# Optimization experiments

Hardware: AMD Instinct MI355X
Metric: run time of the kernel (lower is better)

The kernel has to match this reference:

```python
import jax, jax.numpy as jnp
import numpy as np

L, D, HID, NH, E, K, P, IMG, NC, B = 4, 384, 1536, 6, 8, 2, 16, 224, 1000, 8
S = (IMG // P) ** 2 + 1  # 197 tokens (cls + patches)
EPS = 1e-5


def setup_inputs() -> dict:
    ks = iter(jax.random.split(jax.random.key(0), 32))
    g = lambda shape, s=0.02: jax.random.normal(next(ks), shape, jnp.float32) * s
    pd = 3 * P * P
    return dict(
        x=jax.random.normal(next(ks), (B, 3, IMG, IMG), jnp.float32),
        patch_w=g((pd, D)), patch_b=g((D,)),
        cls_tok=g((1, 1, D)), pos=g((1, S, D)),
        qkv_w=g((L, D, 3 * D)), qkv_b=g((L, 3 * D)),
        proj_w=g((L, D, D)), proj_b=g((L, D)),
        ln1_g=jnp.ones((L, D)), ln1_b=jnp.zeros((L, D)),
        ln2_g=jnp.ones((L, D)), ln2_b=jnp.zeros((L, D)),
        router_w=g((L, D, E)), router_b=g((L, E)),
        w1=g((L, E, D, HID)), b1=g((L, E, HID)),
        w2=g((L, E, HID, D)), b2=g((L, E, D)),
        norm_g=jnp.ones((D,)), norm_b=jnp.zeros((D,)),
        fc_w=g((D, NC)), fc_b=g((NC,)),
    )


def _ln(x, g, b):
    m = x.mean(-1, keepdims=True)
    v = ((x - m) ** 2).mean(-1, keepdims=True)
    return (x - m) * jax.lax.rsqrt(v + EPS) * g + b


def _mha(x, wqkv, bqkv, wo, bo):
    Bx, Sx, Dx = x.shape
    hd = Dx // NH
    qkv = x @ wqkv + bqkv
    q, k, v = jnp.split(qkv, 3, axis=-1)
    q = q.reshape(Bx, Sx, NH, hd)
    k = k.reshape(Bx, Sx, NH, hd)
    v = v.reshape(Bx, Sx, NH, hd)
    att = jnp.einsum('bqhd,bkhd->bhqk', q, k) / jnp.sqrt(jnp.float32(hd))
    att = jax.nn.softmax(att, axis=-1)
    o = jnp.einsum('bhqk,bkhd->bqhd', att, v).reshape(Bx, Sx, Dx)
    return o @ wo + bo


def _moe(x, rw, rb, w1, b1, w2, b2, noise):
    # Faithful to the masked-dense SparseMoE: non-routed experts see zeros,
    # so occupied experts leak expert_j(0)=gelu(b1_j)@W2_j+b2_j to all tokens.
    xf = x.reshape(-1, x.shape[-1])                     # [T, D]
    logits = xf @ rw + rb + noise * 0.01                # noisy gating
    vals, idx = jax.lax.top_k(logits, K)                # [T, K]
    gates = jax.nn.softmax(vals, axis=-1)               # [T, K]
    h = jax.nn.gelu(jnp.einsum('td,edh->teh', xf, w1) + b1[None], approximate=False)
    y = jnp.einsum('teh,ehd->ted', h, w2) + b2[None]    # [T, E, D]
    bias0 = jnp.einsum('eh,ehd->ed', jax.nn.gelu(b1, approximate=False), w2) + b2  # expert_j(0)
    oh = jax.nn.one_hot(idx, E, dtype=xf.dtype)         # [T, K, E]
    occ = (oh.sum(0) > 0).astype(xf.dtype)              # [K, E] slot occupancy (mask.sum()>0)
    bias_sum = occ @ bias0                              # [K, D]
    y_sel = jnp.take_along_axis(y, idx[:, :, None], axis=1)  # [T, K, D]
    out = jnp.einsum('tk,tkd->td', gates, y_sel - bias0[idx] + bias_sum[None])
    return out.reshape(x.shape)


def reference(x, patch_w, patch_b, cls_tok, pos, qkv_w, qkv_b, proj_w, proj_b,
              ln1_g, ln1_b, ln2_g, ln2_b, router_w, router_b,
              w1, b1, w2, b2, norm_g, norm_b, fc_w, fc_b):
    Bx = x.shape[0]
    Hp = IMG // P
    # torch unfold patchify: (B,C,Hp,Wp,p,p) -> (B, N, C*p*p), channel-major features
    patches = x.reshape(Bx, 3, Hp, P, Hp, P).transpose(0, 2, 4, 1, 3, 5).reshape(Bx, Hp * Hp, 3 * P * P)
    t = patches @ patch_w + patch_b
    t = jnp.concatenate([jnp.broadcast_to(cls_tok, (Bx, 1, D)), t], axis=1) + pos
    nkey = jax.random.key(42)
    for l in range(L):
        a = _mha(t, qkv_w[l], qkv_b[l], proj_w[l], proj_b[l])
        t = _ln(t + a, ln1_g[l], ln1_b[l])
        noise = jax.random.normal(jax.random.fold_in(nkey, l), (Bx * S, E), t.dtype)
        m = _moe(t, router_w[l], router_b[l], w1[l], b1[l], w2[l], b2[l], noise)
        t = _ln(t + m, ln2_g[l], ln2_b[l])
    t = _ln(t, norm_g, norm_b)
    return t[:, 0] @ fc_w + fc_b
```

## Files before the change

kernel.cpp:

```cpp
#include <hip/hip_runtime.h>
#include <hip/hip_bf16.h>

constexpr int LYR  = 4;
constexpr int DM   = 384;
constexpr int HIDN = 1536;
constexpr int NHEAD = 6;
constexpr int HDIM = 64;
constexpr int NEXP = 8;
constexpr int SEQ  = 197;
constexpr int BATCH = 8;
constexpr int TOK  = BATCH * SEQ;
constexpr int NCLS = 1000;
constexpr int CAPE = TOK;
constexpr int NPATCH = BATCH * 196;
constexpr float EPSLN = 1e-5f;
constexpr int KP = 40;

typedef __attribute__((ext_vector_type(8))) short short8v;
typedef __attribute__((ext_vector_type(4))) short short4v;
typedef __attribute__((ext_vector_type(2))) short short2v;
typedef __attribute__((ext_vector_type(4))) float f32x4v;

__host__ __device__ inline void tf2x32(unsigned k0, unsigned k1, unsigned x0, unsigned x1,
                                       unsigned& y0, unsigned& y1) {
  unsigned ks2 = k0 ^ k1 ^ 0x1BD11BDAu;
  unsigned v0 = x0 + k0, v1 = x1 + k1;
#define TFR(r) { v0 += v1; v1 = (v1 << (r)) | (v1 >> (32 - (r))); v1 ^= v0; }
  TFR(13) TFR(15) TFR(26) TFR(6)
  v0 += k1;  v1 += ks2 + 1u;
  TFR(17) TFR(29) TFR(16) TFR(24)
  v0 += ks2; v1 += k0 + 2u;
  TFR(13) TFR(15) TFR(26) TFR(6)
  v0 += k0;  v1 += k1 + 3u;
  TFR(17) TFR(29) TFR(16) TFR(24)
  v0 += k1;  v1 += ks2 + 4u;
  TFR(13) TFR(15) TFR(26) TFR(6)
  v0 += ks2; v1 += k0 + 5u;
#undef TFR
  y0 = v0; y1 = v1;
}

__device__ inline float erfinv32(float x) {
  float w = -log1pf(-x * x);
  float p;
  if (w < 5.f) {
    w -= 2.5f;
    p = 2.81022636e-08f;
    p = fmaf(p, w, 3.43273939e-07f);
    p = fmaf(p, w, -3.5233877e-06f);
    p = fmaf(p, w, -4.39150654e-06f);
    p = fmaf(p, w, 0.00021858087f);
    p = fmaf(p, w, -0.00125372503f);
    p = fmaf(p, w, -0.00417768164f);
    p = fmaf(p, w, 0.246640727f);
    p = fmaf(p, w, 1.50140941f);
  } else {
    w = sqrtf(w) - 3.f;
    p = -0.000200214257f;
    p = fmaf(p, w, 0.000100950558f);
    p = fmaf(p, w, 0.00134934322f);
    p = fmaf(p, w, -0.00367342844f);
    p = fmaf(p, w, 0.00573950773f);
    p = fmaf(p, w, -0.0076224613f);
    p = fmaf(p, w, 0.00943887047f);
    p = fmaf(p, w, 1.00167406f);
    p = fmaf(p, w, 2.83297682f);
  }
  return p * x;
}

__device__ inline float gelu_f(float x) {
  return 0.5f * x * (1.f + erff(x * 0.70710678118654752f));
}

__device__ inline unsigned short bf16_rne(float x) {
  unsigned u = __float_as_uint(x);
  unsigned r = (u + 0x7fffu + ((u >> 16) & 1u)) >> 16;
  return (unsigned short)r;
}
__device__ inline void split2(float x, short& hs, short& ls) {
  unsigned hu = bf16_rne(x);
  float hf = __uint_as_float(hu << 16);
  unsigned lu = bf16_rne(x - hf);
  hs = (short)hu; ls = (short)lu;
}

__global__ __launch_bounds__(256) void convw_kernel(const float* __restrict__ src,
                                                    short* __restrict__ dst,
                                                    int K, int N) {
  const int nchunks = (K >> 5) * (N >> 4);
  const int chunk = blockIdx.x * 4 + (threadIdx.x >> 6);
  if (chunk >= nchunks) return;
  const int lane = threadIdx.x & 63;
  const long eoffS = (long)blockIdx.y * K * N;
  const long eoffD = (long)blockIdx.y * nchunks * 1024;
  const int nc = N >> 4;
  const int kt = chunk / nc, nt = chunk - kt * nc;
  const int n = nt * 16 + (lane & 15);
  const int kb = kt * 32 + (lane >> 4) * 8;
  short8v hv, lv;
#pragma unroll
  for (int j = 0; j < 8; j++) {
    short h, l;
    split2(src[eoffS + (long)(kb + j) * N + n], h, l);
    hv[j] = h; lv[j] = l;
  }
  *(short8v*)&dst[eoffD + (long)chunk * 1024 + lane * 8] = hv;
  *(short8v*)&dst[eoffD + (long)chunk * 1024 + 512 + lane * 8] = lv;
}

template <int KTOT, int NTOT, int MODE>
__global__ __launch_bounds__(256) void gemm_lds_kernel(
    const short* __restrict__ Ah, const short* __restrict__ Al,
    const short* __restrict__ Wf, const float* __restrict__ bias,
    const int* __restrict__ lists, const int* __restrict__ counts,
    float* __restrict__ outF, short* __restrict__ outH, short* __restrict__ outL) {
  constexpr bool ISMOE = (MODE == 1 || MODE == 2);
  constexpr bool SPLITOUT = (MODE == 1 || MODE == 3);
  constexpr int SPE = NTOT / 64;
  constexpr int NK = KTOT / 32;
  constexpr int PIT = 36;
  const int strip = blockIdx.x;
  int e, c0;
  if (ISMOE) { e = strip / SPE; c0 = (strip - e * SPE) * 64; }
  else { e = 0; c0 = strip * 64; if (c0 >= NTOT) return; }
  const int m = blockIdx.y;
  const int cnt = ISMOE ? counts[e] : TOK;
  if (m * 64 >= cnt) return;
  const int rowsM = min(64, cnt - m * 64);
  __shared__ int ent[64];
  __shared__ short sh[2][64 * PIT];
  __shared__ short sl[2][64 * PIT];
  const int tid = threadIdx.x;
  const int w = tid >> 6, lane = tid & 63;
  if (ISMOE) {
    if (tid < 64) ent[tid] = (tid < rowsM) ? lists[e * CAPE + m * 64 + tid] : -1;
    __syncthreads();
  }
  const int sr = tid >> 2, skq = (tid & 3) * 8;
  bool okr; long arow = 0;
  if (!ISMOE) {
    okr = (sr < rowsM);
    arow = (long)(m * 64 + (okr ? sr : 0)) * KTOT;
  } else {
    const int pid = ent[sr];
    okr = (pid >= 0);
    arow = (long)(okr ? ((MODE == 1) ? (pid >> 1) : pid) : 0) * KTOT;
  }
  const short* W = Wf + (long)e * ((KTOT >> 5) * (NTOT >> 4)) * 1024;
  const int wm = (w >> 1) * 32, wn = (w & 1) * 32;
  f32x4v Cr[2][2] = {};
  short8v ch, cl;
#pragma unroll
  for (int j = 0; j < 8; j++) { ch[j] = 0; cl[j] = 0; }
  if (okr) {
    ch = *(const short8v*)&Ah[arow + skq];
    cl = *(const short8v*)&Al[arow + skq];
  }
#pragma unroll 2
  for (int kt = 0; kt < NK; ++kt) {
    const int cb = kt & 1;
    *(short8v*)&sh[cb][sr * PIT + skq] = ch;
    *(short8v*)&sl[cb][sr * PIT + skq] = cl;
    if (kt + 1 < NK && okr) {
      ch = *(const short8v*)&Ah[arow + (kt + 1) * 32 + skq];
      cl = *(const short8v*)&Al[arow + (kt + 1) * 32 + skq];
    }
    const long wkb = ((long)kt * (NTOT >> 4) + (c0 >> 4) + (wn >> 4)) * 1024;
    short8v wh[2], wl[2];
#pragma unroll
    for (int nt = 0; nt < 2; ++nt) {
      wh[nt] = *(const short8v*)&W[wkb + nt * 1024 + lane * 8];
      wl[nt] = *(const short8v*)&W[wkb + nt * 1024 + 512 + lane * 8];
    }
    __syncthreads();
    short8v bh[2], bl[2];
#pragma unroll
    for (int tt = 0; tt < 2; ++tt) {
      const int trow = wm + tt * 16 + (lane & 15);
      bh[tt] = *(const short8v*)&sh[cb][trow * PIT + (lane >> 4) * 8];
      bl[tt] = *(const short8v*)&sl[cb][trow * PIT + (lane >> 4) * 8];
    }
#pragma unroll
    for (int nt = 0; nt < 2; ++nt) {
#pragma unroll
      for (int tt = 0; tt < 2; ++tt) {
        Cr[tt][nt] = __builtin_amdgcn_mfma_f32_16x16x32_bf16(wh[nt], bh[tt], Cr[tt][nt], 0, 0, 0);
        Cr[tt][nt] = __builtin_amdgcn_mfma_f32_16x16x32_bf16(wh[nt], bl[tt], Cr[tt][nt], 0, 0, 0);
        Cr[tt][nt] = __builtin_amdgcn_mfma_f32_16x16x32_bf16(wl[nt], bh[tt], Cr[tt][nt], 0, 0, 0);
      }
    }
  }
  const int tl = lane & 15;
  const int nq = (lane >> 4) * 4;
#pragma unroll
  for (int tt = 0; tt < 2; ++tt) {
    const int trow = wm + tt * 16 + tl;
    if (trow < rowsM) {
      const long orow = (long)(ISMOE ? ent[trow] : (m * 64 + trow)) * NTOT;
#pragma unroll
      for (int nt = 0; nt < 2; ++nt) {
        const int n = c0 + wn + nt * 16 + nq;
        const float4 bv = *(const float4*)&bias[(ISMOE ? e * NTOT : 0) + n];
        float o0 = Cr[tt][nt][0] + bv.x, o1 = Cr[tt][nt][1] + bv.y;
        float o2 = Cr[tt][nt][2] + bv.z, o3 = Cr[tt][nt][3] + bv.w;
        if (SPLITOUT) {
          if (MODE == 1) { o0 = gelu_f(o0); o1 = gelu_f(o1); o2 = gelu_f(o2); o3 = gelu_f(o3); }
          short4v hv, lv; short hs, ls;
          split2(o0, hs, ls); hv[0] = hs; lv[0] = ls;
          split2(o1, hs, ls); hv[1] = hs; lv[1] = ls;
          split2(o2, hs, ls); hv[2] = hs; lv[2] = ls;
          split2(o3, hs, ls); hv[3] = hs; lv[3] = ls;
          *(short4v*)&outH[orow + n] = hv;
          *(short4v*)&outL[orow + n] = lv;
        } else {
          *(float4*)&outF[orow + n] = make_float4(o0, o1, o2, o3);
        }
      }
    }
  }
}

__global__ __launch_bounds__(256) void patch_mfma_kernel(const float* __restrict__ x,
                                                         const short* __restrict__ Wf,
                                                         const float* __restrict__ pb,
                                                         const float* __restrict__ pos,
                                                         float* __restrict__ t,
                                                         short* __restrict__ tfh,
                                                         short* __restrict__ tfl) {
  constexpr int KTOT = 768, NTOT = DM;
  const int rowsM = min(64, NPATCH - (int)blockIdx.x * 64);
  const int c0 = blockIdx.z * 64;
  const int tid = threadIdx.x;
  const int w = tid >> 6, lane = tid & 63;
  __shared__ short xh[64 * KP];
  __shared__ short xl[64 * KP];
  const int sr = tid >> 2, skq = (tid & 3) * 8;
  const bool okr = (sr < rowsM);
  const int p = blockIdx.x * 64 + sr;
  const int pbat = okr ? (p / 196) : 0;
  const int pn = okr ? (p - pbat * 196) : 0;
  const int hp = pn / 14, wp = pn - hp * 14;
  const float* xbase = x + ((long)pbat * 3 * 224 + hp * 16) * 224 + wp * 16;
  const int wm = (w >> 1) * 32, wn = (w & 1) * 32;
  f32x4v Cr[2][2] = {};
  float4 ra = make_float4(0.f, 0.f, 0.f, 0.f), rb = ra;
  if (okr) {
    const int f = skq;
    const int c = f >> 8, py = (f >> 4) & 15, px = f & 15;
    const float* ptr = xbase + ((long)c * 224 + py) * 224 + px;
    ra = *(const float4*)ptr;
    rb = *(const float4*)(ptr + 4);
  }
  for (int kt = 0; kt < KTOT / 32; ++kt) {
    __syncthreads();
    {
      const float v[8] = {ra.x, ra.y, ra.z, ra.w, rb.x, rb.y, rb.z, rb.w};
      short8v hv, lv;
#pragma unroll
      for (int j = 0; j < 8; j++) { short h, l; split2(v[j], h, l); hv[j] = h; lv[j] = l; }
      *(short8v*)&xh[sr * KP + skq] = hv;
      *(short8v*)&xl[sr * KP + skq] = lv;
    }
    if (kt + 1 < KTOT / 32 && okr) {
      const int f = (kt + 1) * 32 + skq;
      const int c = f >> 8, py = (f >> 4) & 15, px = f & 15;
      const float* ptr = xbase + ((long)c * 224 + py) * 224 + px;
      ra = *(const float4*)ptr;
      rb = *(const float4*)(ptr + 4);
    }
    __syncthreads();
    short8v bhv[2], blv[2];
#pragma unroll
    for (int tt = 0; tt < 2; ++tt) {
      const int trow = wm + tt * 16 + (lane & 15);
      bhv[tt] = *(const short8v*)&xh[trow * KP + (lane >> 4) * 8];
      blv[tt] = *(const short8v*)&xl[trow * KP + (lane >> 4) * 8];
    }
    const long wkb = ((long)kt * (NTOT >> 4) + (c0 >> 4) + (wn >> 4)) * 1024;
#pragma unroll
    for (int nt = 0; nt < 2; ++nt) {
      const short8v wh = *(const short8v*)&Wf[wkb + nt * 1024 + lane * 8];
      const short8v wl = *(const short8v*)&Wf[wkb + nt * 1024 + 512 + lane * 8];
#pragma unroll
      for (int tt = 0; tt < 2; ++tt) {
        Cr[tt][nt] = __builtin_amdgcn_mfma_f32_16x16x32_bf16(wh, bhv[tt], Cr[tt][nt], 0, 0, 0);
        Cr[tt][nt] = __builtin_amdgcn_mfma_f32_16x16x32_bf16(wh, blv[tt], Cr[tt][nt], 0, 0, 0);
        Cr[tt][nt] = __builtin_amdgcn_mfma_f32_16x16x32_bf16(wl, bhv[tt], Cr[tt][nt], 0, 0, 0);
      }
    }
  }
  const int tl = lane & 15;
  const int nq = (lane >> 4) * 4;
#pragma unroll
  for (int tt = 0; tt < 2; ++tt) {
    const int trow = wm + tt * 16 + tl;
    if (trow < rowsM) {
      const int r = blockIdx.x * 64 + trow;
      const int b2 = r / 196, n2 = r - b2 * 196;
      const long orow = (long)(b2 * SEQ + 1 + n2) * DM;
#pragma unroll
      for (int nt = 0; nt < 2; ++nt) {
        const int n = c0 + wn + nt * 16 + nq;
        const float4 bv = *(const float4*)&pb[n];
        const float4 pv = *(const float4*)&pos[(1 + n2) * DM + n];
        float o0 = Cr[tt][nt][0] + bv.x + pv.x;
        float o1 = Cr[tt][nt][1] + bv.y + pv.y;
        float o2 = Cr[tt][nt][2] + bv.z + pv.z;
        float o3 = Cr[tt][nt][3] + bv.w + pv.w;
        *(float4*)&t[orow + n] = make_float4(o0, o1, o2, o3);
        short4v hv, lv; short hs, ls;
        split2(o0, hs, ls); hv[0] = hs; lv[0] = ls;
        split2(o1, hs, ls); hv[1] = hs; lv[1] = ls;
        split2(o2, hs, ls); hv[2] = hs; lv[2] = ls;
        split2(o3, hs, ls); hv[3] = hs; lv[3] = ls;
        *(short4v*)&tfh[orow + n] = hv;
        *(short4v*)&tfl[orow + n] = lv;
      }
    }
  }
}

__global__ void cls_pos_kernel(const float* __restrict__ cls, const float* __restrict__ pos,
                               float* __restrict__ t,
                               short* __restrict__ tfh, short* __restrict__ tfl) {
  int b = blockIdx.x, d = threadIdx.x;
  float v = cls[d] + pos[d];
  t[(b * SEQ) * DM + d] = v;
  short hs, ls; split2(v, hs, ls);
  tfh[(b * SEQ) * DM + d] = hs;
  tfl[(b * SEQ) * DM + d] = ls;
}

constexpr int APIT = 232;
constexpr int VPIT = 40;
__global__ __launch_bounds__(256) void attn_mfma_kernel(const short* __restrict__ qh,
                                                        const short* __restrict__ ql,
                                                        short* __restrict__ afh,
                                                        short* __restrict__ afl) {
  const int bh = blockIdx.x;
  const int b = bh / NHEAD, h = bh % NHEAD;
  const int q0 = blockIdx.y * 64;
  const int tid = threadIdx.x;
  const int w = tid >> 6, lane = tid & 63;
  const int tl = lane & 15, g = lane >> 4;
  __shared__ short ph[4][16 * APIT];
  __shared__ short pl[4][16 * APIT];
  __shared__ short vsh[64 * VPIT];
  __shared__ short vsl[64 * VPIT];
  const long hq = (long)h * HDIM;

  const int qrow = q0 + w * 16 + tl;
  const long qtok = (long)(b * SEQ + min(qrow, SEQ - 1)) * 1152;
  short8v qfh[2], qfl[2];
#pragma unroll
  for (int s = 0; s < 2; ++s) {
    qfh[s] = *(const short8v*)&qh[qtok + hq + s * 32 + g * 8];
    qfl[s] = *(const short8v*)&ql[qtok + hq + s * 32 + g * 8];
  }

  f32x4v sc[13];
#pragma unroll
  for (int n = 0; n < 13; ++n) {
    f32x4v acc = {};
    const long ktok = (long)(b * SEQ + min(n * 16 + tl, SEQ - 1)) * 1152;
#pragma unroll
    for (int s = 0; s < 2; ++s) {
      const short8v kh = *(const short8v*)&qh[ktok + DM + hq + s * 32 + g * 8];
      const short8v kl = *(const short8v*)&ql[ktok + DM + hq + s * 32 + g * 8];
      acc = __builtin_amdgcn_mfma_f32_16x16x32_bf16(kh, qfh[s], acc, 0, 0, 0);
      acc = __builtin_amdgcn_mfma_f32_16x16x32_bf16(kh, qfl[s], acc, 0, 0, 0);
      acc = __builtin_amdgcn_mfma_f32_16x16x32_bf16(kl, qfh[s], acc, 0, 0, 0);
    }
    sc[n] = acc;
  }

  float m = -1e30f;
#pragma unroll
  for (int n = 0; n < 13; ++n)
#pragma unroll
    for (int j = 0; j < 4; ++j) {
      const int key = n * 16 + g * 4 + j;
      float v = sc[n][j] * 0.125f;
      v = (key < SEQ) ? v : -1e30f;
      sc[n][j] = v;
      m = fmaxf(m, v);
    }
  m = fmaxf(m, __shfl_xor(m, 16));
  m = fmaxf(m, __shfl_xor(m, 32));
  float sum = 0.f;
#pragma unroll
  for (int n = 0; n < 13; ++n)
#pragma unroll
    for (int j = 0; j < 4; ++j) {
      float p = __expf(sc[n][j] - m);
      sc[n][j] = p; sum += p;
    }
  sum += __shfl_xor(sum, 16);
  sum += __shfl_xor(sum, 32);
  const float inv = 1.f / sum;

  short* prowh = &ph[w][tl * APIT];
  short* prowl = &pl[w][tl * APIT];
#pragma unroll
  for (int n = 0; n < 13; ++n) {
    short4v hv, lv;
#pragma unroll
    for (int j = 0; j < 4; ++j) {
      short hs, ls; split2(sc[n][j] * inv, hs, ls);
      hv[j] = hs; lv[j] = ls;
    }
    *(short4v*)&prowh[n * 16 + g * 4] = hv;
    *(short4v*)&prowl[n * 16 + g * 4] = lv;
  }
  {
    short4v z; z[0] = 0; z[1] = 0; z[2] = 0; z[3] = 0;
    *(short4v*)&prowh[208 + g * 4] = z;
    *(short4v*)&prowl[208 + g * 4] = z;
  }

  const int kp = (tid & 15) * 2;
  const int dg = (tid >> 4) * 4;
  f32x4v oacc[4] = {};
  short4v r0h, r0l, r1h, r1l;
  {
    const long t0 = (long)(b * SEQ + min(kp, SEQ - 1)) * 1152 + 2 * DM + hq + dg;
    const long t1 = (long)(b * SEQ + min(kp + 1, SEQ - 1)) * 1152 + 2 * DM + hq + dg;
    r0h = *(const short4v*)&qh[t0]; r0l = *(const short4v*)&ql[t0];
    r1h = *(const short4v*)&qh[t1]; r1l = *(const short4v*)&ql[t1];
  }
  for (int st = 0; st < 7; ++st) {
    __syncthreads();
#pragma unroll
    for (int jj = 0; jj < 4; ++jj) {
      short2v h2; h2[0] = r0h[jj]; h2[1] = r1h[jj];
      short2v l2; l2[0] = r0l[jj]; l2[1] = r1l[jj];
      *(short2v*)&vsh[(dg + jj) * VPIT + kp] = h2;
      *(short2v*)&vsl[(dg + jj) * VPIT + kp] = l2;
    }
    if (st + 1 < 7) {
      const int kb = (st + 1) * 32;
      const long t0 = (long)(b * SEQ + min(kb + kp, SEQ - 1)) * 1152 + 2 * DM + hq + dg;
      const long t1 = (long)(b * SEQ + min(kb + kp + 1, SEQ - 1)) * 1152 + 2 * DM + hq + dg;
      r0h = *(const short4v*)&qh[t0]; r0l = *(const short4v*)&ql[t0];
      r1h = *(const short4v*)&qh[t1]; r1l = *(const short4v*)&ql[t1];
    }
    __syncthreads();
    const short8v pbh = *(const short8v*)&prowh[st * 32 + g * 8];
    const short8v pbl = *(const short8v*)&prowl[st * 32 + g * 8];
#pragma unroll
    for (int dt = 0; dt < 4; ++dt) {
      const short8v vfh = *(const short8v*)&vsh[(dt * 16 + tl) * VPIT + g * 8];
      const short8v vfl = *(const short8v*)&vsl[(dt * 16 + tl) * VPIT + g * 8];
      oacc[dt] = __builtin_amdgcn_mfma_f32_16x16x32_bf16(vfh, pbh, oacc[dt], 0, 0, 0);
      oacc[dt] = __builtin_amdgcn_mfma_f32_16x16x32_bf16(vfh, pbl, oacc[dt], 0, 0, 0);
      oacc[dt] = __builtin_amdgcn_mfma_f32_16x16x32_bf16(vfl, pbh, oacc[dt], 0, 0, 0);
    }
  }

  if (qrow < SEQ) {
    const long obase = (long)(b * SEQ + qrow) * DM + hq;
#pragma unroll
    for (int dt = 0; dt < 4; ++dt) {
      short4v hv, lv; short hs, ls;
      split2(oacc[dt][0], hs, ls); hv[0] = hs; lv[0] = ls;
      split2(oacc[dt][1], hs, ls); hv[1] = hs; lv[1] = ls;
      split2(oacc[dt][2], hs, ls); hv[2] = hs; lv[2] = ls;
      split2(oacc[dt][3], hs, ls); hv[3] = hs; lv[3] = ls;
      *(short4v*)&afh[obase + dt * 16 + g * 4] = hv;
      *(short4v*)&afl[obase + dt * 16 + g * 4] = lv;
    }
  }
}

__global__ __launch_bounds__(384) void add_ln_kernel(float* __restrict__ t,
                                                     const float* __restrict__ delta,
                                                     const float* __restrict__ g,
                                                     const float* __restrict__ bta,
                                                     short* __restrict__ tfh,
                                                     short* __restrict__ tfl) {
  int tok = blockIdx.x, d = threadIdx.x;
  float v = t[tok * DM + d] + delta[tok * DM + d];
  float sv = v, sq = v * v;
  for (int off = 32; off > 0; off >>= 1) { sv += __shfl_xor(sv, off); sq += __shfl_xor(sq, off); }
  __shared__ float rs[6], rq[6];
  int w = d >> 6, ln = d & 63;
  if (ln == 0) { rs[w] = sv; rq[w] = sq; }
  __syncthreads();
  float mean = 0.f, ms = 0.f;
#pragma unroll
  for (int i = 0; i < 6; i++) { mean += rs[i]; ms += rq[i]; }
  mean *= (1.f / DM); ms *= (1.f / DM);
  float inv = rsqrtf(ms - mean * mean + EPSLN);
  float y = (v - mean) * inv * g[d] + bta[d];
  t[tok * DM + d] = y;
  short hs, ls; split2(y, hs, ls);
  tfh[tok * DM + d] = hs;
  tfl[tok * DM + d] = ls;
}

__global__ __launch_bounds__(256) void router_logits_kernel(const float* __restrict__ t,
                                                            const float* __restrict__ rw,
                                                            const float* __restrict__ rb,
                                                            unsigned k0, unsigned k1,
                                                            float* __restrict__ gates,
                                                            int* __restrict__ idxb) {
  const int tok = blockIdx.x * 4 + (threadIdx.x >> 6);
  const int lane = threadIdx.x & 63;
  const int e = lane & 7, j = lane >> 3;
  const float* xr = t + tok * DM;
  float acc = 0.f;
  for (int d2 = j * 48; d2 < j * 48 + 48; d2++) acc += xr[d2] * rw[d2 * NEXP + e];
  acc += __shfl_xor(acc, 8);
  acc += __shfl_xor(acc, 16);
  acc += __shfl_xor(acc, 32);
  if (lane < 8) {
    acc += rb[e];
    unsigned i = (unsigned)(tok * NEXP + e);
    unsigned y0, y1;
    tf2x32(k0, k1, 0u, i, y0, y1);
    unsigned bits = y0 ^ y1;
    float f = __uint_as_float(0x3f800000u | (bits >> 9)) - 1.0f;
    const float lo = -0.99999994f;
    float u = f * 2.0f + lo;
    u = fmaxf(lo, u);
    acc += 0.01f * (1.41421356f * erfinv32(u));
  }
  float lg[8];
#pragma unroll
  for (int qq = 0; qq < 8; qq++) lg[qq] = __shfl(acc, qq);
  if (lane == 0) {
    int i0 = 0; float v0 = lg[0];
#pragma unroll
    for (int qq = 1; qq < 8; qq++) if (lg[qq] > v0) { v0 = lg[qq]; i0 = qq; }
    int i1 = -1; float v1 = -1e30f;
#pragma unroll
    for (int qq = 0; qq < 8; qq++) if (qq != i0 && lg[qq] > v1) { v1 = lg[qq]; i1 = qq; }
    float e1 = __expf(v1 - v0);
    float g0 = 1.f / (1.f + e1);
    idxb[tok * 2] = i0; idxb[tok * 2 + 1] = i1;
    gates[tok * 2] = g0; gates[tok * 2 + 1] = 1.f - g0;
  }
}

__global__ __launch_bounds__(1024) void bucket_kernel(const int* __restrict__ idxb,
                                                      int* __restrict__ lists,
                                                      int* __restrict__ counts,
                                                      int* __restrict__ occ) {
  __shared__ int lc[NEXP];
  __shared__ int locc[2 * NEXP];
  const int tid = threadIdx.x;
  if (tid < NEXP) lc[tid] = 0;
  if (tid < 2 * NEXP) locc[tid] = 0;
  __syncthreads();
  for (int i = tid; i < 2 * TOK; i += 1024) {
    const int e = idxb[i];
    const int p = atomicAdd(&lc[e], 1);
    lists[e * CAPE + p] = i;
    locc[(i & 1) * NEXP + e] = 1;
  }
  __syncthreads();
  if (tid < NEXP) counts[tid] = lc[tid];
  if (tid < 2 * NEXP) occ[tid] = locc[tid];
}

__global__ void prep_kernel(const float* __restrict__ b2, float* __restrict__ bias0) {
  int e = blockIdx.x, c = threadIdx.x;
  bias0[e * DM + c] = b2[e * DM + c];
}

__global__ __launch_bounds__(384) void bias0_partial_kernel(const float* __restrict__ b1,
                                                            const float* __restrict__ w2,
                                                            float* __restrict__ bias0) {
  const int e = blockIdx.x, kc = blockIdx.y;
  __shared__ float gb[128];
  const int tid = threadIdx.x;
  if (tid < 128) gb[tid] = gelu_f(b1[e * HIDN + kc * 128 + tid]);
  __syncthreads();
  float acc = 0.f;
  const float* W = w2 + ((long)e * HIDN + kc * 128) * DM + tid;
  for (int j2 = 0; j2 < 128; j2++) acc += gb[j2] * W[(long)j2 * DM];
  atomicAdd(&bias0[e * DM + tid], acc);
}

__global__ __launch_bounds__(384) void bias_sum_kernel(const float* __restrict__ bias0,
                                                       const int* __restrict__ occ,
                                                       float* __restrict__ bias_sum) {
  int k = blockIdx.x, d = threadIdx.x;
  float acc = 0.f;
#pragma unroll
  for (int e = 0; e < NEXP; e++)
    if (occ[k * NEXP + e]) acc += bias0[e * DM + d];
  bias_sum[k * DM + d] = acc;
}

__global__ __launch_bounds__(384) void moe_combine_ln_kernel(float* __restrict__ t,
                                                             const float* __restrict__ ybuf,
                                                             const float* __restrict__ gates,
                                                             const int* __restrict__ idxb,
                                                             const float* __restrict__ bias0,
                                                             const float* __restrict__ bias_sum,
                                                             const float* __restrict__ g,
                                                             const float* __restrict__ bta,
                                                             short* __restrict__ tfh,
                                                             short* __restrict__ tfl) {
  int tok = blockIdx.x, d = threadIdx.x;
  float g0 = gates[tok * 2], g1 = gates[tok * 2 + 1];
  int i0 = idxb[tok * 2], i1 = idxb[tok * 2 + 1];
  float m0 = ybuf[(tok * 2) * DM + d] - bias0[i0 * DM + d] + bias_sum[d];
  float m1 = ybuf[(tok * 2 + 1) * DM + d] - bias0[i1 * DM + d] + bias_sum[DM + d];
  float v = t[tok * DM + d] + g0 * m0 + g1 * m1;
  float sv = v, sq = v * v;
  for (int off = 32; off > 0; off >>= 1) { sv += __shfl_xor(sv, off); sq += __shfl_xor(sq, off); }
  __shared__ float rs[6], rq[6];
  int w = d >> 6, ln = d & 63;
  if (ln == 0) { rs[w] = sv; rq[w] = sq; }
  __syncthreads();
  float mean = 0.f, ms = 0.f;
#pragma unroll
  for (int i = 0; i < 6; i++) { mean += rs[i]; ms += rq[i]; }
  mean *= (1.f / DM); ms *= (1.f / DM);
  float inv = rsqrtf(ms - mean * mean + EPSLN);
  float y = (v - mean) * inv * g[d] + bta[d];
  t[tok * DM + d] = y;
  short hs, ls; split2(y, hs, ls);
  tfh[tok * DM + d] = hs;
  tfl[tok * DM + d] = ls;
}

__global__ __launch_bounds__(256) void final_kernel(const float* __restrict__ t,
                                                    const float* __restrict__ ng,
                                                    const float* __restrict__ nb,
                                                    const float* __restrict__ fw,
                                                    const float* __restrict__ fb,
                                                    float* __restrict__ out) {
  int b = blockIdx.x, chunk = blockIdx.y, tid = threadIdx.x;
  __shared__ float xr[DM];
  __shared__ float rs[4], rq[4];
  const float* row = t + (b * SEQ) * DM;
  float sv = 0.f, sq = 0.f;
  for (int i = tid; i < DM; i += 256) { float x = row[i]; xr[i] = x; sv += x; sq += x * x; }
  for (int off = 32; off > 0; off >>= 1) { sv += __shfl_xor(sv, off); sq += __shfl_xor(sq, off); }
  int w = tid >> 6, ln = tid & 63;
  if (ln == 0) { rs[w] = sv; rq[w] = sq; }
  __syncthreads();
  float mean = (rs[0] + rs[1] + rs[2] + rs[3]) * (1.f / DM);
  float ms = (rq[0] + rq[1] + rq[2] + rq[3]) * (1.f / DM);
  float inv = rsqrtf(ms - mean * mean + EPSLN);
  for (int i = tid; i < DM; i += 256) xr[i] = (xr[i] - mean) * inv * ng[i] + nb[i];
  __syncthreads();
  int c = chunk * 250 + tid;
  if (tid < 250) {
    float acc = fb[c];
    for (int k = 0; k < DM; k++) acc += xr[k] * fw[k * NCLS + c];
    out[b * NCLS + c] = acc;
  }
}

extern "C" void kernel_launch(void* const* d_in, const int* in_sizes, int n_in,
                              void* d_out, int out_size, void* d_ws, size_t ws_size,
                              hipStream_t stream) {
  const float* x       = (const float*)d_in[0];
  const float* patch_w = (const float*)d_in[1];
  const float* patch_b = (const float*)d_in[2];
  const float* cls_tok = (const float*)d_in[3];
  const float* pos     = (const float*)d_in[4];
  const float* qkv_w   = (const float*)d_in[5];
  const float* qkv_b   = (const float*)d_in[6];
  const float* proj_w  = (const float*)d_in[7];
  const float* proj_b  = (const float*)d_in[8];
  const float* ln1_g   = (const float*)d_in[9];
  const float* ln1_b   = (const float*)d_in[10];
  const float* ln2_g   = (const float*)d_in[11];
  const float* ln2_b   = (const float*)d_in[12];
  const float* router_w = (const float*)d_in[13];
  const float* router_b = (const float*)d_in[14];
  const float* w1      = (const float*)d_in[15];
  const float* b1      = (const float*)d_in[16];
  const float* w2      = (const float*)d_in[17];
  const float* b2      = (const float*)d_in[18];
  const float* norm_g  = (const float*)d_in[19];
  const float* norm_b  = (const float*)d_in[20];
  const float* fc_w    = (const float*)d_in[21];
  const float* fc_b    = (const float*)d_in[22];

  float* ws = (float*)d_ws;
  float* t        = ws;
  float* proj     = t + TOK * DM;
  float* ybuf     = proj + TOK * DM;
  float* bias0    = ybuf + TOK * 2 * DM;
  float* bias_sum = bias0 + NEXP * DM;
  float* gates    = bias_sum + 2 * DM;
  int* idxb   = (int*)(gates + TOK * 2);
  int* lists  = idxb + TOK * 2;
  int* counts = lists + NEXP * CAPE;
  int* occ    = counts + NEXP;
  short* tfh = (short*)(occ + 2 * NEXP);
  short* tfl = tfh + TOK * DM;
  short* afh = tfl + TOK * DM;
  short* afl = afh + TOK * DM;
  short* qvh = afl + TOK * DM;
  short* qvl = qvh + TOK * 1152;
  short* hbh = qvl + TOK * 1152;
  short* hbl = hbh + 2 * TOK * HIDN;
  short* wqf = hbl + 2 * TOK * HIDN;
  short* wpf = wqf + 864 * 1024;
  short* w1f = wpf + 288 * 1024;
  short* w2f = w1f + 8 * 1152 * 1024;
  short* wpatf = w2f + 8 * 1152 * 1024;

  convw_kernel<<<dim3(144, 1), 256, 0, stream>>>(patch_w, wpatf, 768, DM);
  patch_mfma_kernel<<<dim3(25, 1, 6), 256, 0, stream>>>(x, wpatf, patch_b, pos, t, tfh, tfl);
  cls_pos_kernel<<<BATCH, DM, 0, stream>>>(cls_tok, pos, t, tfh, tfl);

  for (int l = 0; l < LYR; l++) {
    convw_kernel<<<dim3(216, 1), 256, 0, stream>>>(qkv_w + (long)l * DM * 1152, wqf, DM, 1152);
    convw_kernel<<<dim3(72, 1), 256, 0, stream>>>(proj_w + (long)l * DM * DM, wpf, DM, DM);
    convw_kernel<<<dim3(288, NEXP), 256, 0, stream>>>(w1 + (long)l * NEXP * DM * HIDN, w1f, DM, HIDN);
    convw_kernel<<<dim3(288, NEXP), 256, 0, stream>>>(w2 + (long)l * NEXP * HIDN * DM, w2f, HIDN, DM);

    gemm_lds_kernel<DM, 1152, 3><<<dim3(24, 25), 256, 0, stream>>>(
        tfh, tfl, wqf, qkv_b + l * 1152, nullptr, nullptr, nullptr, qvh, qvl);
    attn_mfma_kernel<<<dim3(BATCH * NHEAD, 4), 256, 0, stream>>>(qvh, qvl, afh, afl);
    gemm_lds_kernel<DM, DM, 0><<<dim3(8, 25), 256, 0, stream>>>(
        afh, afl, wpf, proj_b + l * DM, nullptr, nullptr, proj, nullptr, nullptr);
    add_ln_kernel<<<TOK, DM, 0, stream>>>(t, proj, ln1_g + l * DM, ln1_b + l * DM, tfh, tfl);

    prep_kernel<<<NEXP, DM, 0, stream>>>(b2 + l * NEXP * DM, bias0);
    bias0_partial_kernel<<<dim3(NEXP, 12), 384, 0, stream>>>(
        b1 + l * NEXP * HIDN, w2 + (long)l * NEXP * HIDN * DM, bias0);
    unsigned kl0, kl1;
    tf2x32(0u, 42u, 0u, (unsigned)l, kl0, kl1);
    router_logits_kernel<<<TOK / 4, 256, 0, stream>>>(
        t, router_w + l * DM * NEXP, router_b + l * NEXP, kl0, kl1, gates, idxb);
    bucket_kernel<<<1, 1024, 0, stream>>>(idxb, lists, counts, occ);
    bias_sum_kernel<<<2, 384, 0, stream>>>(bias0, occ, bias_sum);
    gemm_lds_kernel<DM, HIDN, 1><<<dim3(192, 25), 256, 0, stream>>>(
        tfh, tfl, w1f, b1 + l * NEXP * HIDN, lists, counts, nullptr, hbh, hbl);
    gemm_lds_kernel<HIDN, DM, 2><<<dim3(48, 25), 256, 0, stream>>>(
        hbh, hbl, w2f, b2 + l * NEXP * DM, lists, counts, ybuf, nullptr, nullptr);
    moe_combine_ln_kernel<<<TOK, DM, 0, stream>>>(t, ybuf, gates, idxb, bias0, bias_sum,
                                                  ln2_g + l * DM, ln2_b + l * DM, tfh, tfl);
  }

  final_kernel<<<dim3(BATCH, 4), 256, 0, stream>>>(t, norm_g, norm_b, fc_w, fc_b,
                                                   (float*)d_out);
}
```

Measured before the change: 900.9 us.

## Hoist weight conversion out of layer loop, deepen GEMM K-tile, fuse bias_sum

All per-layer weight split/conversion and the bias0 precomputation now run once up front as batched launches over a layer grid dimension, with per-layer workspace slices. This cuts many small kernel launches and dependency stalls inside the layer loop. The GEMM K-tile goes from 32 to 64 per LDS stage, halving the barrier count at the cost of more LDS and registers. bias_sum is folded into bucket_kernel, which removes one launch. The workspace grows to hold all layers' converted weights.

After: 824.3 us. 1.09x faster.

```diff
diff --git a/kernel.cpp b/kernel.cpp
--- a/kernel.cpp
+++ b/kernel.cpp
@@ -87,13 +87,16 @@
 
 __global__ __launch_bounds__(256) void convw_kernel(const float* __restrict__ src,
                                                     short* __restrict__ dst,
-                                                    int K, int N) {
+                                                    int K, int N,
+                                                    long srcLS, long dstLS) {
   const int nchunks = (K >> 5) * (N >> 4);
   const int chunk = blockIdx.x * 4 + (threadIdx.x >> 6);
   if (chunk >= nchunks) return;
   const int lane = threadIdx.x & 63;
-  const long eoffS = (long)blockIdx.y * K * N;
-  const long eoffD = (long)blockIdx.y * nchunks * 1024;
+  const long loS = (long)blockIdx.z * srcLS;
+  const long loD = (long)blockIdx.z * dstLS;
+  const long eoffS = loS + (long)blockIdx.y * K * N;
+  const long eoffD = loD + (long)blockIdx.y * nchunks * 1024;
   const int nc = N >> 4;
   const int kt = chunk / nc, nt = chunk - kt * nc;
   const int n = nt * 16 + (lane & 15);
@@ -118,8 +121,8 @@
   constexpr bool ISMOE = (MODE == 1 || MODE == 2);
   constexpr bool SPLITOUT = (MODE == 1 || MODE == 3);
   constexpr int SPE = NTOT / 64;
-  constexpr int NK = KTOT / 32;
-  constexpr int PIT = 36;
+  constexpr int NK = KTOT / 64;
+  constexpr int PIT = 72;
   const int strip = blockIdx.x;
   int e, c0;
   if (ISMOE) { e = strip / SPE; c0 = (strip - e * SPE) * 64; }
@@ -150,44 +153,56 @@
   const short* W = Wf + (long)e * ((KTOT >> 5) * (NTOT >> 4)) * 1024;
   const int wm = (w >> 1) * 32, wn = (w & 1) * 32;
   f32x4v Cr[2][2] = {};
-  short8v ch, cl;
-#pragma unroll
-  for (int j = 0; j < 8; j++) { ch[j] = 0; cl[j] = 0; }
+  short8v c0h, c1h, c0l, c1l;
+#pragma unroll
+  for (int j = 0; j < 8; j++) { c0h[j] = 0; c1h[j] = 0; c0l[j] = 0; c1l[j] = 0; }
   if (okr) {
-    ch = *(const short8v*)&Ah[arow + skq];
-    cl = *(const short8v*)&Al[arow + skq];
-  }
-#pragma unroll 2
+    c0h = *(const short8v*)&Ah[arow + skq];
+    c1h = *(const short8v*)&Ah[arow + 32 + skq];
+    c0l = *(const short8v*)&Al[arow + skq];
+    c1l = *(const short8v*)&Al[arow + 32 + skq];
+  }
   for (int kt = 0; kt < NK; ++kt) {
     const int cb = kt & 1;
-    *(short8v*)&sh[cb][sr * PIT + skq] = ch;
-    *(short8v*)&sl[cb][sr * PIT + skq] = cl;
+    *(short8v*)&sh[cb][sr * PIT + skq] = c0h;
+    *(short8v*)&sh[cb][sr * PIT + 32 + skq] = c1h;
+    *(short8v*)&sl[cb][sr * PIT + skq] = c0l;
+    *(short8v*)&sl[cb][sr * PIT + 32 + skq] = c1l;
     if (kt + 1 < NK && okr) {
-      ch = *(const short8v*)&Ah[arow + (kt + 1) * 32 + skq];
-      cl = *(const short8v*)&Al[arow + (kt + 1) * 32 + skq];
-    }
-    const long wkb = ((long)kt * (NTOT >> 4) + (c0 >> 4) + (wn >> 4)) * 1024;
-    short8v wh[2], wl[2];
-#pragma unroll
-    for (int nt = 0; nt < 2; ++nt) {
-      wh[nt] = *(const short8v*)&W[wkb + nt * 1024 + lane * 8];
-      wl[nt] = *(const short8v*)&W[wkb + nt * 1024 + 512 + lane * 8];
+      const long ab = arow + (kt + 1) * 64;
+      c0h = *(const short8v*)&Ah[ab + skq];
+      c1h = *(const short8v*)&Ah[ab + 32 + skq];
+      c0l = *(const short8v*)&Al[ab + skq];
+      c1l = *(const short8v*)&Al[ab + 32 + skq];
+    }
+    short8v wh[2][2], wl[2][2];
+#pragma unroll
+    for (int kk = 0; kk < 2; ++kk) {
+      const long wkb = ((long)(kt * 2 + kk) * (NTOT >> 4) + (c0 >> 4) + (wn >> 4)) * 1024;
+#pragma unroll
+      for (int nt = 0; nt < 2; ++nt) {
+        wh[kk][nt] = *(const short8v*)&W[wkb + nt * 1024 + lane * 8];
+        wl[kk][nt] = *(const short8v*)&W[wkb + nt * 1024 + 512 + lane * 8];
+      }
     }
     __syncthreads();
-    short8v bh[2], bl[2];
-#pragma unroll
-    for (int tt = 0; tt < 2; ++tt) {
-      const int trow = wm + tt * 16 + (lane & 15);
-      bh[tt] = *(const short8v*)&sh[cb][trow * PIT + (lane >> 4) * 8];
-      bl[tt] = *(const short8v*)&sl[cb][trow * PIT + (lane >> 4) * 8];
-    }
-#pragma unroll
-    for (int nt = 0; nt < 2; ++nt) {
+#pragma unroll
+    for (int kk = 0; kk < 2; ++kk) {
+      short8v bh[2], bl[2];
 #pragma unroll
       for (int tt = 0; tt < 2; ++tt) {
-        Cr[tt][nt] = __builtin_amdgcn_mfma_f32_16x16x32_bf16(wh[nt], bh[tt], Cr[tt][nt], 0, 0, 0);
-        Cr[tt][nt] = __builtin_amdgcn_mfma_f32_16x16x32_bf16(wh[nt], bl[tt], Cr[tt][nt], 0, 0, 0);
-        Cr[tt][nt] = __builtin_amdgcn_mfma_f32_16x16x32_bf16(wl[nt], bh[tt], Cr[tt][nt], 0, 0, 0);
+        const int trow = wm + tt * 16 + (lane & 15);
+        bh[tt] = *(const short8v*)&sh[cb][trow * PIT + kk * 32 + (lane >> 4) * 8];
+        bl[tt] = *(const short8v*)&sl[cb][trow * PIT + kk * 32 + (lane >> 4) * 8];
+      }
+#pragma unroll
+      for (int nt = 0; nt < 2; ++nt) {
+#pragma unroll
+        for (int tt = 0; tt < 2; ++tt) {
+          Cr[tt][nt] = __builtin_amdgcn_mfma_f32_16x16x32_bf16(wh[kk][nt], bh[tt], Cr[tt][nt], 0, 0, 0);
+          Cr[tt][nt] = __builtin_amdgcn_mfma_f32_16x16x32_bf16(wh[kk][nt], bl[tt], Cr[tt][nt], 0, 0, 0);
+          Cr[tt][nt] = __builtin_amdgcn_mfma_f32_16x16x32_bf16(wl[kk][nt], bh[tt], Cr[tt][nt], 0, 0, 0);
+        }
       }
     }
   }
@@ -546,7 +561,8 @@
 __global__ __launch_bounds__(1024) void bucket_kernel(const int* __restrict__ idxb,
                                                       int* __restrict__ lists,
                                                       int* __restrict__ counts,
-                                                      int* __restrict__ occ) {
+                                                      const float* __restrict__ bias0,
+                                                      float* __restrict__ bias_sum) {
   __shared__ int lc[NEXP];
   __shared__ int locc[2 * NEXP];
   const int tid = threadIdx.x;
@@ -561,37 +577,33 @@
   }
   __syncthreads();
   if (tid < NEXP) counts[tid] = lc[tid];
-  if (tid < 2 * NEXP) occ[tid] = locc[tid];
+  if (tid < 2 * DM) {
+    const int k = tid / DM, d = tid - k * DM;
+    float acc = 0.f;
+#pragma unroll
+    for (int e = 0; e < NEXP; e++)
+      if (locc[k * NEXP + e]) acc += bias0[e * DM + d];
+    bias_sum[k * DM + d] = acc;
+  }
 }
 
 __global__ void prep_kernel(const float* __restrict__ b2, float* __restrict__ bias0) {
-  int e = blockIdx.x, c = threadIdx.x;
-  bias0[e * DM + c] = b2[e * DM + c];
+  const long i = ((long)blockIdx.y * NEXP + blockIdx.x) * DM + threadIdx.x;
+  bias0[i] = b2[i];
 }
 
 __global__ __launch_bounds__(384) void bias0_partial_kernel(const float* __restrict__ b1,
                                                             const float* __restrict__ w2,
                                                             float* __restrict__ bias0) {
-  const int e = blockIdx.x, kc = blockIdx.y;
+  const int e = blockIdx.x, kc = blockIdx.y, l = blockIdx.z;
   __shared__ float gb[128];
   const int tid = threadIdx.x;
-  if (tid < 128) gb[tid] = gelu_f(b1[e * HIDN + kc * 128 + tid]);
+  if (tid < 128) gb[tid] = gelu_f(b1[(long)l * NEXP * HIDN + e * HIDN + kc * 128 + tid]);
   __syncthreads();
   float acc = 0.f;
-  const float* W = w2 + ((long)e * HIDN + kc * 128) * DM + tid;
+  const float* W = w2 + ((long)l * NEXP * HIDN + (long)e * HIDN + kc * 128) * DM + tid;
   for (int j2 = 0; j2 < 128; j2++) acc += gb[j2] * W[(long)j2 * DM];
-  atomicAdd(&bias0[e * DM + tid], acc);
-}
-
-__global__ __launch_bounds__(384) void bias_sum_kernel(const float* __restrict__ bias0,
-                                                       const int* __restrict__ occ,
-                                                       float* __restrict__ bias_sum) {
-  int k = blockIdx.x, d = threadIdx.x;
-  float acc = 0.f;
-#pragma unroll
-  for (int e = 0; e < NEXP; e++)
-    if (occ[k * NEXP + e]) acc += bias0[e * DM + d];
-  bias_sum[k * DM + d] = acc;
+  atomicAdd(&bias0[((long)l * NEXP + e) * DM + tid], acc);
 }
 
 __global__ __launch_bounds__(384) void moe_combine_ln_kernel(float* __restrict__ t,
@@ -689,13 +701,12 @@
   float* proj     = t + TOK * DM;
   float* ybuf     = proj + TOK * DM;
   float* bias0    = ybuf + TOK * 2 * DM;
-  float* bias_sum = bias0 + NEXP * DM;
+  float* bias_sum = bias0 + LYR * NEXP * DM;
   float* gates    = bias_sum + 2 * DM;
   int* idxb   = (int*)(gates + TOK * 2);
   int* lists  = idxb + TOK * 2;
   int* counts = lists + NEXP * CAPE;
-  int* occ    = counts + NEXP;
-  short* tfh = (short*)(occ + 2 * NEXP);
+  short* tfh = (short*)(counts + 8);
   short* tfl = tfh + TOK * DM;
   short* afh = tfl + TOK * DM;
   short* afl = afh + TOK * DM;
@@ -704,42 +715,52 @@
   short* hbh = qvl + TOK * 1152;
   short* hbl = hbh + 2 * TOK * HIDN;
   short* wqf = hbl + 2 * TOK * HIDN;
-  short* wpf = wqf + 864 * 1024;
-  short* w1f = wpf + 288 * 1024;
-  short* w2f = w1f + 8 * 1152 * 1024;
-  short* wpatf = w2f + 8 * 1152 * 1024;
-
-  convw_kernel<<<dim3(144, 1), 256, 0, stream>>>(patch_w, wpatf, 768, DM);
+  short* wpf = wqf + (long)LYR * 864 * 1024;
+  short* w1f = wpf + (long)LYR * 288 * 1024;
+  short* w2f = w1f + (long)LYR * NEXP * 1152 * 1024;
+  short* wpatf = w2f + (long)LYR * NEXP * 1152 * 1024;
+
+  convw_kernel<<<dim3(144, 1, 1), 256, 0, stream>>>(patch_w, wpatf, 768, DM, 0, 0);
+  convw_kernel<<<dim3(216, 1, LYR), 256, 0, stream>>>(qkv_w, wqf, DM, 1152,
+                                                      (long)DM * 1152, 864L * 1024);
+  convw_kernel<<<dim3(72, 1, LYR), 256, 0, stream>>>(proj_w, wpf, DM, DM,
+                                                     (long)DM * DM, 288L * 1024);
+  convw_kernel<<<dim3(288, NEXP, LYR), 256, 0, stream>>>(w1, w1f, DM, HIDN,
+                                                         (long)NEXP * DM * HIDN,
+                                                         (long)NEXP * 1152 * 1024);
+  convw_kernel<<<dim3(288, NEXP, LYR), 256, 0, stream>>>(w2, w2f, HIDN, DM,
+                                                         (long)NEXP * HIDN * DM,
+                                                         (long)NEXP * 1152 * 1024);
+  prep_kernel<<<dim3(NEXP, LYR), DM, 0, stream>>>(b2, bias0);
+  bias0_partial_kernel<<<dim3(NEXP, 12, LYR), 384, 0, stream>>>(b1, w2, bias0);
+
   patch_mfma_kernel<<<dim3(25, 1, 6), 256, 0, stream>>>(x, wpatf, patch_b, pos, t, tfh, tfl);
   cls_pos_kernel<<<BATCH, DM, 0, stream>>>(cls_tok, pos, t, tfh, tfl);
 
   for (int l = 0; l < LYR; l++) {
-    convw_kernel<<<dim3(216, 1), 256, 0, stream>>>(qkv_w + (long)l * DM * 1152, wqf, DM, 1152);
-    convw_kernel<<<dim3(72, 1), 256, 0, stream>>>(proj_w + (long)l * DM * DM, wpf, DM, DM);
-    convw_kernel<<<dim3(288, NEXP), 256, 0, stream>>>(w1 + (long)l * NEXP * DM * HIDN, w1f, DM, HIDN);
-    convw_kernel<<<dim3(288, NEXP), 256, 0, stream>>>(w2 + (long)l * NEXP * HIDN * DM, w2f, HIDN, DM);
+    const short* wqf_l = wqf + (long)l * 864 * 1024;
+    const short* wpf_l = wpf + (long)l * 288 * 1024;
+    const short* w1f_l = w1f + (long)l * NEXP * 1152 * 1024;
+    const short* w2f_l = w2f + (long)l * NEXP * 1152 * 1024;
+    const float* bias0_l = bias0 + (long)l * NEXP * DM;
 
     gemm_lds_kernel<DM, 1152, 3><<<dim3(24, 25), 256, 0, stream>>>(
-        tfh, tfl, wqf, qkv_b + l * 1152, nullptr, nullptr, nullptr, qvh, qvl);
+        tfh, tfl, wqf_l, qkv_b + l * 1152, nullptr, nullptr, nullptr, qvh, qvl);
     attn_mfma_kernel<<<dim3(BATCH * NHEAD, 4), 256, 0, stream>>>(qvh, qvl, afh, afl);
     gemm_lds_kernel<DM, DM, 0><<<dim3(8, 25), 256, 0, stream>>>(
-        afh, afl, wpf, proj_b + l * DM, nullptr, nullptr, proj, nullptr, nullptr);
+        afh, afl, wpf_l, proj_b + l * DM, nullptr, nullptr, proj, nullptr, nullptr);
     add_ln_kernel<<<TOK, DM, 0, stream>>>(t, proj, ln1_g + l * DM, ln1_b + l * DM, tfh, tfl);
 
-    prep_kernel<<<NEXP, DM, 0, stream>>>(b2 + l * NEXP * DM, bias0);
-    bias0_partial_kernel<<<dim3(NEXP, 12), 384, 0, stream>>>(
-        b1 + l * NEXP * HIDN, w2 + (long)l * NEXP * HIDN * DM, bias0);
     unsigned kl0, kl1;
     tf2x32(0u, 42u, 0u, (unsigned)l, kl0, kl1);
     router_logits_kernel<<<TOK / 4, 256, 0, stream>>>(
         t, router_w + l * DM * NEXP, router_b + l * NEXP, kl0, kl1, gates, idxb);
-    bucket_kernel<<<1, 1024, 0, stream>>>(idxb, lists, counts, occ);
-    bias_sum_kernel<<<2, 384, 0, stream>>>(bias0, occ, bias_sum);
+    bucket_kernel<<<1, 1024, 0, stream>>>(idxb, lists, counts, bias0_l, bias_sum);
     gemm_lds_kernel<DM, HIDN, 1><<<dim3(192, 25), 256, 0, stream>>>(
-        tfh, tfl, w1f, b1 + l * NEXP * HIDN, lists, counts, nullptr, hbh, hbl);
+        tfh, tfl, w1f_l, b1 + l * NEXP * HIDN, lists, counts, nullptr, hbh, hbl);
     gemm_lds_kernel<HIDN, DM, 2><<<dim3(48, 25), 256, 0, stream>>>(
-        hbh, hbl, w2f, b2 + l * NEXP * DM, lists, counts, ybuf, nullptr, nullptr);
-    moe_combine_ln_kernel<<<TOK, DM, 0, stream>>>(t, ybuf, gates, idxb, bias0, bias_sum,
+        hbh, hbl, w2f_l, b2 + l * NEXP * DM, lists, counts, ybuf, nullptr, nullptr);
+    moe_combine_ln_kernel<<<TOK, DM, 0, stream>>>(t, ybuf, gates, idxb, bias0_l, bias_sum,
                                                   ln2_g + l * DM, ln2_b + l * DM, tfh, tfl);
   }
 
```
